# Kernel optimization log

Measured on AMD Instinct MI355X. Metric: run time of the kernel, lower is better.

## Reference

```python
import jax, jax.numpy as jnp
import numpy as np

H = 16  # number of heads

def setup_inputs() -> dict:
    key = jax.random.key(0)
    ks = jax.random.split(key, 9)
    B, N, D = 2, 2048, 1024
    s = 0.02
    q = jax.random.normal(ks[0], (B, N, D), jnp.float32)
    k = jax.random.normal(ks[1], (B, N, D), jnp.float32)
    v = jax.random.normal(ks[2], (B, N, D), jnp.float32)
    mask = jax.random.randint(ks[3], (B, 1, N, N), 0, 2).astype(bool)
    Wq = jax.random.normal(ks[4], (D, D), jnp.float32) * s
    Wk = jax.random.normal(ks[5], (D, D), jnp.float32) * s
    Wv = jax.random.normal(ks[6], (D, D), jnp.float32) * s
    Wo = jax.random.normal(ks[7], (D, D), jnp.float32) * s
    bq = jnp.zeros((D,), jnp.float32)
    bk = jnp.zeros((D,), jnp.float32)
    bv = jnp.zeros((D,), jnp.float32)
    bo = jnp.zeros((D,), jnp.float32)
    return {"q": q, "k": k, "v": v, "mask": mask,
            "Wq": Wq, "bq": bq, "Wk": Wk, "bk": bk,
            "Wv": Wv, "bv": bv, "Wo": Wo, "bo": bo}


def reference(q, k, v, mask, Wq, bq, Wk, bk, Wv, bv, Wo, bo):
    B, N, D = q.shape
    dk = D // H
    # nn.Linear: x @ W.T + b, then split heads: b n (h d) -> b h n d
    def proj(x, W, b):
        return (x @ W.T + b).reshape(B, N, H, dk).transpose(0, 2, 1, 3)
    qh = proj(q, Wq, bq)  # [B,H,N,dk]
    kh = proj(k, Wk, bk)
    vh = proj(v, Wv, bv)
    # NOTE: original has NO 1/sqrt(dk) scaling
    score = jnp.einsum('bhnd,bhmd->bhnm', qh, kh)
    score = jnp.where(mask, jnp.float32(-1e9), score)
    attn = jax.nn.softmax(score, axis=-1)
    x = jnp.einsum('bhnm,bhmd->bhnd', attn, vh)
    x = x.transpose(0, 2, 1, 3).reshape(B, N, D)  # b h n d -> b n (h d)
    return x @ Wo.T + bo
```

## Files before the change

kernel.cpp:

```cpp
#include <hip/hip_runtime.h>
#include <math.h>

#define BB 2
#define NN 2048
#define DD 1024
#define HH 16
#define DK 64
#define LOG2E 1.4426950408889634f

typedef __attribute__((ext_vector_type(8))) short short8;
typedef __attribute__((ext_vector_type(4))) float f32x4;
typedef __attribute__((ext_vector_type(16))) float f32x16;
typedef __attribute__((ext_vector_type(4))) float f32x4v;
typedef __attribute__((ext_vector_type(8))) unsigned short ushort8;
typedef unsigned long long u64;

__device__ __forceinline__ unsigned short f2bf(float f) {
  unsigned u = __float_as_uint(f);
  unsigned r = (u + 0x7FFFu + ((u >> 16) & 1u)) >> 16;
  return (unsigned short)r;
}

__device__ __forceinline__ unsigned cvtpk(float a, float b) {
  unsigned r;
  asm("v_cvt_pk_bf16_f32 %0, %1, %2" : "=v"(r) : "v"(a), "v"(b));
  return r;
}

__device__ __forceinline__ void gload_lds16(const void* g, void* l) {
  auto gp = (const __attribute__((address_space(1))) unsigned int*)(unsigned long long)g;
  auto lp = (__attribute__((address_space(3))) unsigned int*)(unsigned int)(unsigned long long)l;
  __builtin_amdgcn_global_load_lds(gp, lp, 16, 0, 0);
}

__global__ __launch_bounds__(256) void cvt_w(
    const float* __restrict__ wq, const float* __restrict__ wk, const float* __restrict__ wv,
    const float* __restrict__ wo, unsigned short* __restrict__ ws)
{
  const long NW = (long)DD * DD;
  long i = ((long)blockIdx.x * blockDim.x + threadIdx.x) * 8;
  if (i >= 4 * NW) return;
  int s = (int)(i / NW);
  const float* src = (s == 0) ? wq : (s == 1) ? wk : (s == 2) ? wv : wo;
  long off = i - (long)s * NW;
  unsigned short* dst = ws + (long)s * NW + off;
  f32x4v a = *(const f32x4v*)(src + off);
  f32x4v b = *(const f32x4v*)(src + off + 4);
  ushort8 o;
  o[0] = f2bf(a[0]); o[1] = f2bf(a[1]); o[2] = f2bf(a[2]); o[3] = f2bf(a[3]);
  o[4] = f2bf(b[0]); o[5] = f2bf(b[1]); o[6] = f2bf(b[2]); o[7] = f2bf(b[3]);
  *(ushort8*)dst = o;
}

__global__ __launch_bounds__(256) void cvt_mask_bits(const void* __restrict__ mask,
                                                     u64* __restrict__ mb, long total64)
{
  const unsigned char* m8 = (const unsigned char*)mask;
  const int l = threadIdx.x & 63;
  unsigned probe = m8[l * 4 + 1] | m8[l * 4 + 2] | m8[l * 4 + 3];
  const bool isBool = (__any(probe != 0) != 0);

  long t = (long)blockIdx.x * blockDim.x + threadIdx.x;
  if (t >= total64) return;
  u64 bits = 0;
  if (isBool) {
    const uint4* p = (const uint4*)(m8 + t * 64);
#pragma unroll
    for (int i = 0; i < 4; ++i) {
      uint4 q4 = p[i];
      unsigned vv[4] = {q4.x, q4.y, q4.z, q4.w};
#pragma unroll
      for (int j = 0; j < 4; ++j)
#pragma unroll
        for (int bb = 0; bb < 4; ++bb)
          bits |= (u64)((vv[j] >> (8 * bb)) & 1u) << (i * 16 + j * 4 + bb);
    }
  } else {
    const int4* p = (const int4*)((const int*)mask + t * 64);
#pragma unroll
    for (int i = 0; i < 16; ++i) {
      int4 q4 = p[i];
      bits |= (u64)(q4.x & 1) << (i * 4);
      bits |= (u64)(q4.y & 1) << (i * 4 + 1);
      bits |= (u64)(q4.z & 1) << (i * 4 + 2);
      bits |= (u64)(q4.w & 1) << (i * 4 + 3);
    }
  }
  const long bb2 = t >> 16;
  const long qq = (t >> 5) & 2047;
  const long tcol = t & 31;
  mb[(bb2 * 32 + tcol) * 2048 + qq] = bits;
}

struct GemmArgs {
  const void* A;
  const unsigned short* Bw;
  const float* bias;
  void* C;
  int mode;
  float oscale;
};

template<int TM, int BN, int AFP32>
__global__ __launch_bounds__(256) void gemm_bt(GemmArgs ga0, GemmArgs ga1, GemmArgs ga2)
{
  constexpr int K = DD;
  constexpr int Nn = DD;
  constexpr int GX = 1024 / BN;
  constexpr int GY = 4096 / TM;
  constexpr int PERZ = GX * GY;
  constexpr int MF = TM / 32;
  constexpr int NF = BN / 32;
  constexpr int NT = K / 32;
  __shared__ __align__(16) unsigned short As[3][TM * 32];
  __shared__ __align__(16) unsigned short Bs[3][BN * 32];

  int wgid = blockIdx.x + (blockIdx.y + blockIdx.z * GY) * GX;
  const int nwg = (int)gridDim.z * PERZ;
  const int chunk = nwg >> 3;
  wgid = (wgid & 7) * chunk + (wgid >> 3);
  const int zi = wgid / PERZ;
  const int rem = wgid % PERZ;
  const int m0 = (rem / GX) * TM;
  const int n0 = (rem % GX) * BN;
  GemmArgs ga = (zi == 0) ? ga0 : ((zi == 1) ? ga1 : ga2);

  const int tid = threadIdx.x;
  const int lane = tid & 63;
  const int w = tid >> 6;
  const int m_woff = (w >> 1) * (TM / 2);
  const int n_woff = (w & 1) * (BN / 2);
  const int c = lane & 15, g = lane >> 4;

  f32x4 acc[MF][NF];
  const f32x4 z4 = {0.f, 0.f, 0.f, 0.f};
#pragma unroll
  for (int m = 0; m < MF; ++m)
#pragma unroll
    for (int n = 0; n < NF; ++n) acc[m][n] = z4;

  const unsigned short* Bb = ga.Bw + (long)n0 * K;
  const int ar = tid >> 2;
  const int ac = ((tid & 3) ^ (ar & 3)) * 8;

  auto STAGE_B = [&](int buf, int kk) {
#pragma unroll
    for (int i = 0; i < BN / 64; ++i)
      gload_lds16(Bb + (long)(i * 64 + ar) * K + kk + ac, &Bs[buf][i * 2048 + tid * 8]);
  };

  const unsigned short* Ab16 = (const unsigned short*)ga.A + (long)m0 * K;
  const int arow = tid >> 1;
  const int ahalf = tid & 1;
  const float* Afp = (const float*)ga.A + (long)(m0 + arow) * K + ahalf * 16;
  f32x4v areg[4];

  auto STAGE_A16 = [&](int buf, int kk) {
#pragma unroll
    for (int i = 0; i < TM / 64; ++i)
      gload_lds16(Ab16 + (long)(i * 64 + ar) * K + kk + ac, &As[buf][i * 2048 + tid * 8]);
  };
  auto LOAD_A = [&](int kk) {
#pragma unroll
    for (int j = 0; j < 4; ++j) areg[j] = *(const f32x4v*)(Afp + kk + 4 * j);
  };
  auto WRITE_A = [&](int buf) {
    union { short8 s; unsigned u[4]; } p0, p1;
#pragma unroll
    for (int k = 0; k < 4; ++k) p0.u[k] = cvtpk(areg[k >> 1][(k & 1) * 2], areg[k >> 1][(k & 1) * 2 + 1]);
#pragma unroll
    for (int k = 0; k < 4; ++k) p1.u[k] = cvtpk(areg[(k + 4) >> 1][(k & 1) * 2], areg[(k + 4) >> 1][(k & 1) * 2 + 1]);
    const int G0 = (2 * ahalf) ^ (arow & 3);
    const int G1 = (2 * ahalf + 1) ^ (arow & 3);
    *(short8*)((char*)&As[buf][0] + arow * 64 + G0 * 16) = p0.s;
    *(short8*)((char*)&As[buf][0] + arow * 64 + G1 * 16) = p1.s;
  };

  if constexpr (AFP32) {
    LOAD_A(0);
    STAGE_B(0, 0);
    WRITE_A(0);
    LOAD_A(32);
    STAGE_B(1, 32);
  } else {
    STAGE_A16(0, 0);
    STAGE_B(0, 0);
    STAGE_A16(1, 32);
    STAGE_B(1, 32);
  }

  const int rswz = (g ^ (c & 3)) * 8;

  for (int t = 0; t < NT; ++t) {
    if constexpr (AFP32) {
      if (t < NT - 1) asm volatile("s_waitcnt vmcnt(2)" ::: "memory");
      else            asm volatile("s_waitcnt vmcnt(0)" ::: "memory");
    } else {
      constexpr int LPS = TM / 64 + BN / 64;
      if (t < NT - 1) {
        if constexpr (LPS == 4) asm volatile("s_waitcnt vmcnt(4)" ::: "memory");
        else                    asm volatile("s_waitcnt vmcnt(3)" ::: "memory");
      } else {
        asm volatile("s_waitcnt vmcnt(0)" ::: "memory");
      }
    }
    __builtin_amdgcn_s_barrier();
    __builtin_amdgcn_sched_barrier(0);

    if constexpr (AFP32) {
      if (t + 1 < NT) WRITE_A((t + 1) % 3);
      if (t + 2 < NT) { LOAD_A((t + 2) * 32); STAGE_B((t + 2) % 3, (t + 2) * 32); }
    } else {
      if (t + 2 < NT) { STAGE_A16((t + 2) % 3, (t + 2) * 32); STAGE_B((t + 2) % 3, (t + 2) * 32); }
    }

    const int cb = t % 3;
    short8 a[MF], b[NF];
#pragma unroll
    for (int m = 0; m < MF; ++m)
      a[m] = *(const short8*)&As[cb][(m_woff + 16 * m + c) * 32 + rswz];
#pragma unroll
    for (int n = 0; n < NF; ++n)
      b[n] = *(const short8*)&Bs[cb][(n_woff + 16 * n + c) * 32 + rswz];
    __builtin_amdgcn_s_setprio(1);
#pragma unroll
    for (int m = 0; m < MF; ++m)
#pragma unroll
      for (int n = 0; n < NF; ++n)
        acc[m][n] = __builtin_amdgcn_mfma_f32_16x16x32_bf16(a[m], b[n], acc[m][n], 0, 0, 0);
    __builtin_amdgcn_s_setprio(0);
  }

#pragma unroll
  for (int n = 0; n < NF; ++n) {
    const int col = n0 + n_woff + 16 * n + c;
    const float bv = ga.bias[col];
#pragma unroll
    for (int m = 0; m < MF; ++m) {
      const int row0 = m0 + m_woff + 16 * m + 4 * g;
#pragma unroll
      for (int r = 0; r < 4; ++r) {
        const int row = row0 + r;
        const float val = (acc[m][n][r] + bv) * ga.oscale;
        if (ga.mode == 1)
          ((float*)ga.C)[(long)row * Nn + col] = val;
        else if (ga.mode == 0)
          ((unsigned short*)ga.C)[(long)row * Nn + col] = f2bf(val);
        else
          ((unsigned short*)ga.C)[((long)(row >> 11) * DD + col) * NN + (row & (NN - 1))] = f2bf(val);
      }
    }
  }
}

__global__ __launch_bounds__(256, 2) void attn_kernel(
    const unsigned short* __restrict__ Q,
    const unsigned short* __restrict__ K,
    const unsigned short* __restrict__ Vt,
    const u64* __restrict__ mb64,
    unsigned short* __restrict__ ctx)
{
  __shared__ __align__(16) unsigned short Ks[2][64 * 64];
  __shared__ __align__(16) unsigned short Vs[2][64 * 64];

  const int tid = threadIdx.x;
  const int lane = tid & 63;
  const int w = tid >> 6;
  const int bid = blockIdx.x;
  const int b = (bid >> 4) & 1, h = bid & 15;
  const int q0 = (bid >> 5) * 128;
  const int l31 = lane & 31;
  const int hi = lane >> 5;
  const int qrow = q0 + 32 * w + l31;

  short8 aq[4];
  {
    const unsigned short* qp = Q + ((long)(b * NN + qrow)) * DD + h * DK + 8 * hi;
    aq[0] = *(const short8*)(qp);
    aq[1] = *(const short8*)(qp + 16);
    aq[2] = *(const short8*)(qp + 32);
    aq[3] = *(const short8*)(qp + 48);
  }

  f32x16 o0, o1, cinit;
#pragma unroll
  for (int r = 0; r < 16; ++r) { o0[r] = 0.f; o1[r] = 0.f; cinit[r] = -28.853901f; }
  float ls0 = 0.f, ls1 = 0.f;

  const unsigned short* Kbase = K + (long)(b * NN) * DD + h * DK;
  const unsigned short* Vbase = Vt + ((long)(b * DD + h * DK)) * NN;
  const u64* mbase = mb64 + (long)(b * 32) * 2048 + qrow;

  const int srow = tid >> 3;
  const int scol = tid & 7;
  const int swcol = scol ^ (srow & 7);

  auto STAGE = [&](int buf, int t) {
#pragma unroll
    for (int hf = 0; hf < 2; ++hf) {
      const int row = srow + 32 * hf;
      gload_lds16(Kbase + (long)(t * 64 + row) * DD + swcol * 8, &Ks[buf][hf * 2048 + tid * 8]);
      gload_lds16(Vbase + (long)row * NN + t * 64 + swcol * 8, &Vs[buf][hf * 2048 + tid * 8]);
    }
  };

  int koffs[8], voff0[4], voff1[4];
#pragma unroll
  for (int sub = 0; sub < 2; ++sub) {
    const int krow = l31 + 32 * sub;
    const int kswz = (l31 & 7) << 3;
#pragma unroll
    for (int i = 0; i < 4; ++i)
      koffs[sub * 4 + i] = krow * 64 + ((16 * i + 8 * hi) ^ kswz);
#pragma unroll
    for (int dblk = 0; dblk < 2; ++dblk) {
      const int vrow = l31 + 32 * dblk;
      voff0[sub * 2 + dblk] = vrow * 64 + ((32 * sub + 8 * hi) ^ kswz);
      voff1[sub * 2 + dblk] = vrow * 64 + ((32 * sub + 16 + 8 * hi) ^ kswz);
    }
  }

  STAGE(0, 0);
  __syncthreads();
  int cur = 0;
  const int sh4 = 4 * hi;
  u64 mword = mbase[0];

  for (int t = 0; t < 32; ++t) {
    const u64 mnext = (t < 31) ? mbase[(long)(t + 1) * 2048] : 0;
    if (t < 31) STAGE(cur ^ 1, t + 1);
    const unsigned msk0 = ((unsigned)mword) >> sh4;
    const unsigned msk1 = ((unsigned)(mword >> 32)) >> sh4;

#pragma unroll
    for (int sub = 0; sub < 2; ++sub) {
      const unsigned m = sub ? msk1 : msk0;

      f32x16 ss = cinit;
      __builtin_amdgcn_s_setprio(1);
#pragma unroll
      for (int i = 0; i < 4; ++i) {
        const short8 kf = *(const short8*)&Ks[cur][koffs[sub * 4 + i]];
        ss = __builtin_amdgcn_mfma_f32_32x32x16_bf16(kf, aq[i], ss, 0, 0, 0);
      }
      __builtin_amdgcn_s_setprio(0);

      float p[16];
      float lacc = 0.f;
#pragma unroll
      for (int r = 0; r < 16; ++r) {
        const int cr = (r & 3) + 8 * (r >> 2);
        const float e = ((m >> cr) & 1u) ? -1e9f : ss[r];
        p[r] = __builtin_amdgcn_exp2f(e);
        lacc += p[r];
      }
      if (sub == 0) ls0 += lacc; else ls1 += lacc;

      unsigned wv[8];
#pragma unroll
      for (int i = 0; i < 8; ++i) wv[i] = cvtpk(p[2 * i], p[2 * i + 1]);
      asm("v_permlane32_swap_b32 %0, %1" : "+v"(wv[0]), "+v"(wv[2]));
      asm("v_permlane32_swap_b32 %0, %1" : "+v"(wv[1]), "+v"(wv[3]));
      asm("v_permlane32_swap_b32 %0, %1" : "+v"(wv[4]), "+v"(wv[6]));
      asm("v_permlane32_swap_b32 %0, %1" : "+v"(wv[5]), "+v"(wv[7]));
      union { short8 s; unsigned u[4]; } pa0, pa1;
      pa0.u[0] = wv[0]; pa0.u[1] = wv[1]; pa0.u[2] = wv[2]; pa0.u[3] = wv[3];
      pa1.u[0] = wv[4]; pa1.u[1] = wv[5]; pa1.u[2] = wv[6]; pa1.u[3] = wv[7];

      __builtin_amdgcn_s_setprio(1);
      {
        const short8 vb00 = *(const short8*)&Vs[cur][voff0[sub * 2 + 0]];
        const short8 vb10 = *(const short8*)&Vs[cur][voff1[sub * 2 + 0]];
        o0 = __builtin_amdgcn_mfma_f32_32x32x16_bf16(pa0.s, vb00, o0, 0, 0, 0);
        o0 = __builtin_amdgcn_mfma_f32_32x32x16_bf16(pa1.s, vb10, o0, 0, 0, 0);
        const short8 vb01 = *(const short8*)&Vs[cur][voff0[sub * 2 + 1]];
        const short8 vb11 = *(const short8*)&Vs[cur][voff1[sub * 2 + 1]];
        o1 = __builtin_amdgcn_mfma_f32_32x32x16_bf16(pa0.s, vb01, o1, 0, 0, 0);
        o1 = __builtin_amdgcn_mfma_f32_32x32x16_bf16(pa1.s, vb11, o1, 0, 0, 0);
      }
      __builtin_amdgcn_s_setprio(0);
    }
    __syncthreads();
    cur ^= 1;
    mword = mnext;
  }

  float lsum = ls0 + ls1;
  lsum += __shfl_xor(lsum, 32);
  const float inv = 1.0f / lsum;

#pragma unroll
  for (int r = 0; r < 16; ++r) {
    const int qr = (r & 3) + 8 * (r >> 2) + 4 * hi;
    const float linv = __shfl(inv, qr);
    const long row = (long)(b * NN + q0 + 32 * w + qr);
    ctx[row * DD + h * DK + l31] = f2bf(o0[r] * linv);
    ctx[row * DD + h * DK + 32 + l31] = f2bf(o1[r] * linv);
  }
}

extern "C" void kernel_launch(void* const* d_in, const int* in_sizes, int n_in,
                              void* d_out, int out_size, void* d_ws, size_t ws_size,
                              hipStream_t stream) {
  const float* q  = (const float*)d_in[0];
  const float* k  = (const float*)d_in[1];
  const float* v  = (const float*)d_in[2];
  const void*  mask = d_in[3];
  const float* Wq = (const float*)d_in[4];
  const float* bq = (const float*)d_in[5];
  const float* Wk = (const float*)d_in[6];
  const float* bk = (const float*)d_in[7];
  const float* Wv = (const float*)d_in[8];
  const float* bv = (const float*)d_in[9];
  const float* Wo = (const float*)d_in[10];
  const float* bo = (const float*)d_in[11];

  unsigned short* ws = (unsigned short*)d_ws;
  const long NW = (long)DD * DD;
  const long NX = (long)BB * NN * DD;
  unsigned short* Wqb = ws;
  unsigned short* Wkb = ws + NW;
  unsigned short* Wvb = ws + 2 * NW;
  unsigned short* Wob = ws + 3 * NW;
  unsigned short* Qh  = ws + 4 * NW;
  unsigned short* Kh  = Qh + NX;
  unsigned short* Vtr = Kh + NX;
  unsigned short* Ctx = Vtr + NX;
  u64* Mbits = (u64*)(Ctx + NX);
  const long NM64 = (long)BB * NN * NN / 64;

  cvt_w<<<2048, 256, 0, stream>>>(Wq, Wk, Wv, Wo, ws);
  cvt_mask_bits<<<(int)(NM64 / 256), 256, 0, stream>>>(mask, Mbits, NM64);

  GemmArgs gq = {q, Wqb, bq, (void*)Qh, 0, LOG2E};
  GemmArgs gk = {k, Wkb, bk, (void*)Kh, 0, 1.0f};
  GemmArgs gv = {v, Wvb, bv, (void*)Vtr, 2, 1.0f};
  dim3 gproj(DD / 128, (BB * NN) / 128, 3);
  gemm_bt<128, 128, 1><<<gproj, 256, 0, stream>>>(gq, gk, gv);

  attn_kernel<<<512, 256, 0, stream>>>(Qh, Kh, Vtr, Mbits, Ctx);

  GemmArgs go = {Ctx, Wob, bo, d_out, 1, 1.0f};
  dim3 gout(DD / 128, (BB * NN) / 64, 1);
  gemm_bt<64, 128, 0><<<gout, 256, 0, stream>>>(go, go, go);
}
```

Baseline: 141.8 us.

## Split attention KV loop across two wave groups; deepen GEMM A-prefetch pipeline

The attention kernel now runs 512 threads per block. Two groups of four waves each process half of the 32 key/value tiles, staged together. The partial outputs and row sums are then combined through LDS before normalization, which raises per-block parallelism over the sequential KV loop at the cost of more LDS and an extra reduction. The projection GEMM gains a second register bank so fp32 A tiles are loaded three steps ahead, with an adjusted LDS swizzle for the A tile. The transposed V output is written as packed 4-element stores.

```diff
diff --git a/kernel.cpp b/kernel.cpp
--- a/kernel.cpp
+++ b/kernel.cpp
@@ -13,6 +13,7 @@
 typedef __attribute__((ext_vector_type(16))) float f32x16;
 typedef __attribute__((ext_vector_type(4))) float f32x4v;
 typedef __attribute__((ext_vector_type(8))) unsigned short ushort8;
+typedef __attribute__((ext_vector_type(4))) unsigned short ushort4v;
 typedef unsigned long long u64;
 
 __device__ __forceinline__ unsigned short f2bf(float f) {
@@ -153,35 +154,37 @@
   const int arow = tid >> 1;
   const int ahalf = tid & 1;
   const float* Afp = (const float*)ga.A + (long)(m0 + arow) * K + ahalf * 16;
-  f32x4v areg[4];
+  f32x4v aregA[4], aregB[4];
 
   auto STAGE_A16 = [&](int buf, int kk) {
 #pragma unroll
     for (int i = 0; i < TM / 64; ++i)
       gload_lds16(Ab16 + (long)(i * 64 + ar) * K + kk + ac, &As[buf][i * 2048 + tid * 8]);
   };
-  auto LOAD_A = [&](int kk) {
-#pragma unroll
-    for (int j = 0; j < 4; ++j) areg[j] = *(const f32x4v*)(Afp + kk + 4 * j);
-  };
-  auto WRITE_A = [&](int buf) {
+  auto LOAD_A = [&](int kk, f32x4v (&arr)[4]) {
+#pragma unroll
+    for (int j = 0; j < 4; ++j) arr[j] = *(const f32x4v*)(Afp + kk + 4 * j);
+  };
+  auto WRITE_A = [&](int buf, f32x4v (&arr)[4]) {
     union { short8 s; unsigned u[4]; } p0, p1;
-#pragma unroll
-    for (int k = 0; k < 4; ++k) p0.u[k] = cvtpk(areg[k >> 1][(k & 1) * 2], areg[k >> 1][(k & 1) * 2 + 1]);
-#pragma unroll
-    for (int k = 0; k < 4; ++k) p1.u[k] = cvtpk(areg[(k + 4) >> 1][(k & 1) * 2], areg[(k + 4) >> 1][(k & 1) * 2 + 1]);
-    const int G0 = (2 * ahalf) ^ (arow & 3);
-    const int G1 = (2 * ahalf + 1) ^ (arow & 3);
+    p0.u[0] = cvtpk(arr[0][0], arr[0][1]); p0.u[1] = cvtpk(arr[0][2], arr[0][3]);
+    p0.u[2] = cvtpk(arr[1][0], arr[1][1]); p0.u[3] = cvtpk(arr[1][2], arr[1][3]);
+    p1.u[0] = cvtpk(arr[2][0], arr[2][1]); p1.u[1] = cvtpk(arr[2][2], arr[2][3]);
+    p1.u[2] = cvtpk(arr[3][0], arr[3][1]); p1.u[3] = cvtpk(arr[3][2], arr[3][3]);
+    const int fa = ((arow & 1) << 1) | ((arow >> 1) & 1);
+    const int G0 = (2 * ahalf) ^ fa;
+    const int G1 = (2 * ahalf + 1) ^ fa;
     *(short8*)((char*)&As[buf][0] + arow * 64 + G0 * 16) = p0.s;
     *(short8*)((char*)&As[buf][0] + arow * 64 + G1 * 16) = p1.s;
   };
 
   if constexpr (AFP32) {
-    LOAD_A(0);
+    LOAD_A(0, aregA);
+    LOAD_A(32, aregB);
     STAGE_B(0, 0);
-    WRITE_A(0);
-    LOAD_A(32);
     STAGE_B(1, 32);
+    WRITE_A(0, aregA);
+    LOAD_A(64, aregA);
   } else {
     STAGE_A16(0, 0);
     STAGE_B(0, 0);
@@ -190,11 +193,14 @@
   }
 
   const int rswz = (g ^ (c & 3)) * 8;
-
-  for (int t = 0; t < NT; ++t) {
+  const int aswz = AFP32 ? (g ^ (((c & 1) << 1) | ((c >> 1) & 1))) * 8
+                         : rswz;
+
+  auto ITER = [&](int t, f32x4v (&bank)[4]) {
     if constexpr (AFP32) {
-      if (t < NT - 1) asm volatile("s_waitcnt vmcnt(2)" ::: "memory");
-      else            asm volatile("s_waitcnt vmcnt(0)" ::: "memory");
+      if (t < NT - 2)       asm volatile("s_waitcnt vmcnt(6) lgkmcnt(0)" ::: "memory");
+      else if (t == NT - 2) asm volatile("s_waitcnt vmcnt(2) lgkmcnt(0)" ::: "memory");
+      else                  asm volatile("s_waitcnt vmcnt(0) lgkmcnt(0)" ::: "memory");
     } else {
       constexpr int LPS = TM / 64 + BN / 64;
       if (t < NT - 1) {
@@ -208,8 +214,9 @@
     __builtin_amdgcn_sched_barrier(0);
 
     if constexpr (AFP32) {
-      if (t + 1 < NT) WRITE_A((t + 1) % 3);
-      if (t + 2 < NT) { LOAD_A((t + 2) * 32); STAGE_B((t + 2) % 3, (t + 2) * 32); }
+      if (t + 1 < NT) WRITE_A((t + 1) % 3, bank);
+      if (t + 3 < NT) LOAD_A((t + 3) * 32, bank);
+      if (t + 2 < NT) STAGE_B((t + 2) % 3, (t + 2) * 32);
     } else {
       if (t + 2 < NT) { STAGE_A16((t + 2) % 3, (t + 2) * 32); STAGE_B((t + 2) % 3, (t + 2) * 32); }
     }
@@ -218,7 +225,7 @@
     short8 a[MF], b[NF];
 #pragma unroll
     for (int m = 0; m < MF; ++m)
-      a[m] = *(const short8*)&As[cb][(m_woff + 16 * m + c) * 32 + rswz];
+      a[m] = *(const short8*)&As[cb][(m_woff + 16 * m + c) * 32 + aswz];
 #pragma unroll
     for (int n = 0; n < NF; ++n)
       b[n] = *(const short8*)&Bs[cb][(n_woff + 16 * n + c) * 32 + rswz];
@@ -229,6 +236,11 @@
       for (int n = 0; n < NF; ++n)
         acc[m][n] = __builtin_amdgcn_mfma_f32_16x16x32_bf16(a[m], b[n], acc[m][n], 0, 0, 0);
     __builtin_amdgcn_s_setprio(0);
+  };
+
+  for (int t = 0; t < NT; t += 2) {
+    ITER(t, aregB);
+    ITER(t + 1, aregA);
   }
 
 #pragma unroll
@@ -238,40 +250,49 @@
 #pragma unroll
     for (int m = 0; m < MF; ++m) {
       const int row0 = m0 + m_woff + 16 * m + 4 * g;
-#pragma unroll
-      for (int r = 0; r < 4; ++r) {
-        const int row = row0 + r;
-        const float val = (acc[m][n][r] + bv) * ga.oscale;
-        if (ga.mode == 1)
-          ((float*)ga.C)[(long)row * Nn + col] = val;
-        else if (ga.mode == 0)
-          ((unsigned short*)ga.C)[(long)row * Nn + col] = f2bf(val);
-        else
-          ((unsigned short*)ga.C)[((long)(row >> 11) * DD + col) * NN + (row & (NN - 1))] = f2bf(val);
+      if (ga.mode == 2) {
+        ushort4v pk;
+#pragma unroll
+        for (int r = 0; r < 4; ++r) pk[r] = f2bf((acc[m][n][r] + bv) * ga.oscale);
+        *(ushort4v*)&((unsigned short*)ga.C)[((long)(row0 >> 11) * DD + col) * NN + (row0 & (NN - 1))] = pk;
+      } else {
+#pragma unroll
+        for (int r = 0; r < 4; ++r) {
+          const int row = row0 + r;
+          const float val = (acc[m][n][r] + bv) * ga.oscale;
+          if (ga.mode == 1)
+            ((float*)ga.C)[(long)row * Nn + col] = val;
+          else
+            ((unsigned short*)ga.C)[(long)row * Nn + col] = f2bf(val);
+        }
       }
     }
   }
 }
 
-__global__ __launch_bounds__(256, 2) void attn_kernel(
+__global__ __launch_bounds__(512, 4) void attn_kernel(
     const unsigned short* __restrict__ Q,
     const unsigned short* __restrict__ K,
     const unsigned short* __restrict__ Vt,
     const u64* __restrict__ mb64,
     unsigned short* __restrict__ ctx)
 {
-  __shared__ __align__(16) unsigned short Ks[2][64 * 64];
-  __shared__ __align__(16) unsigned short Vs[2][64 * 64];
+  __shared__ __align__(16) char lds_raw[65536];
+  unsigned short* KsB = (unsigned short*)lds_raw;
+  unsigned short* VsB = (unsigned short*)(lds_raw + 32768);
+  float* OB = (float*)lds_raw;
 
   const int tid = threadIdx.x;
   const int lane = tid & 63;
   const int w = tid >> 6;
+  const int grp = w >> 2;
+  const int wq = w & 3;
   const int bid = blockIdx.x;
   const int b = (bid >> 4) & 1, h = bid & 15;
   const int q0 = (bid >> 5) * 128;
   const int l31 = lane & 31;
   const int hi = lane >> 5;
-  const int qrow = q0 + 32 * w + l31;
+  const int qrow = q0 + 32 * wq + l31;
 
   short8 aq[4];
   {
@@ -296,12 +317,10 @@
   const int swcol = scol ^ (srow & 7);
 
   auto STAGE = [&](int buf, int t) {
-#pragma unroll
-    for (int hf = 0; hf < 2; ++hf) {
-      const int row = srow + 32 * hf;
-      gload_lds16(Kbase + (long)(t * 64 + row) * DD + swcol * 8, &Ks[buf][hf * 2048 + tid * 8]);
-      gload_lds16(Vbase + (long)row * NN + t * 64 + swcol * 8, &Vs[buf][hf * 2048 + tid * 8]);
-    }
+    gload_lds16(Kbase + (long)(t * 64 + srow) * DD + swcol * 8, &KsB[buf * 4096 + tid * 8]);
+    gload_lds16(Vbase + (long)srow * NN + t * 64 + swcol * 8, &VsB[buf * 4096 + tid * 8]);
+    gload_lds16(Kbase + (long)((t + 16) * 64 + srow) * DD + swcol * 8, &KsB[(2 + buf) * 4096 + tid * 8]);
+    gload_lds16(Vbase + (long)srow * NN + (t + 16) * 64 + swcol * 8, &VsB[(2 + buf) * 4096 + tid * 8]);
   };
 
   int koffs[8], voff0[4], voff1[4];
@@ -324,13 +343,16 @@
   __syncthreads();
   int cur = 0;
   const int sh4 = 4 * hi;
-  u64 mword = mbase[0];
-
-  for (int t = 0; t < 32; ++t) {
-    const u64 mnext = (t < 31) ? mbase[(long)(t + 1) * 2048] : 0;
-    if (t < 31) STAGE(cur ^ 1, t + 1);
+  u64 mword = mbase[(long)(grp * 16) * 2048];
+
+  for (int t = 0; t < 16; ++t) {
+    const int tt = grp * 16 + t;
+    const u64 mnext = (t < 15) ? mbase[(long)(tt + 1) * 2048] : 0;
+    if (t < 15) STAGE(cur ^ 1, t + 1);
     const unsigned msk0 = ((unsigned)mword) >> sh4;
     const unsigned msk1 = ((unsigned)(mword >> 32)) >> sh4;
+    const unsigned short* Kt = &KsB[(grp * 2 + cur) * 4096];
+    const unsigned short* Vtl = &VsB[(grp * 2 + cur) * 4096];
 
 #pragma unroll
     for (int sub = 0; sub < 2; ++sub) {
@@ -340,7 +362,7 @@
       __builtin_amdgcn_s_setprio(1);
 #pragma unroll
       for (int i = 0; i < 4; ++i) {
-        const short8 kf = *(const short8*)&Ks[cur][koffs[sub * 4 + i]];
+        const short8 kf = *(const short8*)&Kt[koffs[sub * 4 + i]];
         ss = __builtin_amdgcn_mfma_f32_32x32x16_bf16(kf, aq[i], ss, 0, 0, 0);
       }
       __builtin_amdgcn_s_setprio(0);
@@ -369,12 +391,12 @@
 
       __builtin_amdgcn_s_setprio(1);
       {
-        const short8 vb00 = *(const short8*)&Vs[cur][voff0[sub * 2 + 0]];
-        const short8 vb10 = *(const short8*)&Vs[cur][voff1[sub * 2 + 0]];
+        const short8 vb00 = *(const short8*)&Vtl[voff0[sub * 2 + 0]];
+        const short8 vb10 = *(const short8*)&Vtl[voff1[sub * 2 + 0]];
         o0 = __builtin_amdgcn_mfma_f32_32x32x16_bf16(pa0.s, vb00, o0, 0, 0, 0);
         o0 = __builtin_amdgcn_mfma_f32_32x32x16_bf16(pa1.s, vb10, o0, 0, 0, 0);
-        const short8 vb01 = *(const short8*)&Vs[cur][voff0[sub * 2 + 1]];
-        const short8 vb11 = *(const short8*)&Vs[cur][voff1[sub * 2 + 1]];
+        const short8 vb01 = *(const short8*)&Vtl[voff0[sub * 2 + 1]];
+        const short8 vb11 = *(const short8*)&Vtl[voff1[sub * 2 + 1]];
         o1 = __builtin_amdgcn_mfma_f32_32x32x16_bf16(pa0.s, vb01, o1, 0, 0, 0);
         o1 = __builtin_amdgcn_mfma_f32_32x32x16_bf16(pa1.s, vb11, o1, 0, 0, 0);
       }
@@ -386,16 +408,30 @@
   }
 
   float lsum = ls0 + ls1;
-  lsum += __shfl_xor(lsum, 32);
-  const float inv = 1.0f / lsum;
-
-#pragma unroll
-  for (int r = 0; r < 16; ++r) {
-    const int qr = (r & 3) + 8 * (r >> 2) + 4 * hi;
-    const float linv = __shfl(inv, qr);
-    const long row = (long)(b * NN + q0 + 32 * w + qr);
-    ctx[row * DD + h * DK + l31] = f2bf(o0[r] * linv);
-    ctx[row * DD + h * DK + 32 + l31] = f2bf(o1[r] * linv);
+  const int li = wq * 64 + lane;
+  if (grp == 1) {
+    float* dst = OB + (long)li * 33;
+#pragma unroll
+    for (int r = 0; r < 16; ++r) { dst[r] = o0[r]; dst[16 + r] = o1[r]; }
+    dst[32] = lsum;
+  }
+  __syncthreads();
+  if (grp == 0) {
+    const float* src = OB + (long)li * 33;
+#pragma unroll
+    for (int r = 0; r < 16; ++r) { o0[r] += src[r]; o1[r] += src[16 + r]; }
+    lsum += src[32];
+    lsum += __shfl_xor(lsum, 32);
+    const float inv = 1.0f / lsum;
+
+#pragma unroll
+    for (int r = 0; r < 16; ++r) {
+      const int qr = (r & 3) + 8 * (r >> 2) + 4 * hi;
+      const float linv = __shfl(inv, qr);
+      const long row = (long)(b * NN + q0 + 32 * wq + qr);
+      ctx[row * DD + h * DK + l31] = f2bf(o0[r] * linv);
+      ctx[row * DD + h * DK + 32 + l31] = f2bf(o1[r] * linv);
+    }
   }
 }
 
@@ -438,7 +474,7 @@
   dim3 gproj(DD / 128, (BB * NN) / 128, 3);
   gemm_bt<128, 128, 1><<<gproj, 256, 0, stream>>>(gq, gk, gv);
 
-  attn_kernel<<<512, 256, 0, stream>>>(Qh, Kh, Vtr, Mbits, Ctx);
+  attn_kernel<<<512, 512, 0, stream>>>(Qh, Kh, Vtr, Mbits, Ctx);
 
   GemmArgs go = {Ctx, Wob, bo, d_out, 1, 1.0f};
   dim3 gout(DD / 128, (BB * NN) / 64, 1);
```

Result: slower. 289.3 us (+103.9%).
